# Optimization experiments

Hardware: AMD Instinct MI355X
Metric: run time of the kernel (lower is better)

The kernel has to match this reference:

```python
import jax, jax.numpy as jnp
import numpy as np

B, N, E = 8, 4096, 131072
F_IN, F_OUT = 64, 64
ALPHA = 0.2  # LeakyReLU negative slope


def setup_inputs() -> dict:
    key = jax.random.key(0)
    k1, k2, k3, k4, k5 = jax.random.split(key, 5)
    h = jax.random.normal(k1, (B, N, F_IN), dtype=jnp.float32)
    edge_index = jax.random.randint(k2, (2, E), 0, N)
    edge_weight = jax.random.uniform(k3, (E,), dtype=jnp.float32)
    # learned params: Linear weight (no bias) and attention vector a (2*F_OUT, 1)
    W = jax.random.normal(k4, (F_IN, F_OUT), dtype=jnp.float32) / np.sqrt(F_IN)
    a = jax.random.normal(k5, (2 * F_OUT, 1), dtype=jnp.float32) * 0.1
    return {"h": h, "edge_index": edge_index, "edge_weight": edge_weight, "W": W, "a": a}


def _gat_forward(h, edge_weight, W, a, src, dst):
    # Wh: (B, N, F')
    Wh = jnp.einsum("bnf,fo->bno", h, W)
    a1, a2 = a[:F_OUT, 0], a[F_OUT:, 0]
    # score decomposition: [Wh_src || Wh_dst] @ a == Wh_src@a1 + Wh_dst@a2
    s_src = Wh @ a1  # (B, N)
    s_dst = Wh @ a2  # (B, N)
    e = s_src[:, src] + s_dst[:, dst]           # (B, E)
    e = jnp.where(e > 0, e, ALPHA * e)          # LeakyReLU
    e = e * edge_weight[None, :]
    # sparse row-softmax over dst, grouped by src (equals dense masked softmax)
    eT = e.T                                     # (E, B)
    m = jax.ops.segment_max(eT, src, num_segments=N)   # (N, B)
    m = jnp.where(jnp.isfinite(m), m, 0.0)       # rows with no edges
    ex = jnp.exp(eT - m[src])                    # (E, B)
    denom = jax.ops.segment_sum(ex, src, num_segments=N)  # (N, B)
    attn = ex / denom[src]                       # (E, B); denom>0 wherever an edge exists
    # aggregate: h'[b, i] = sum_{e: src[e]=i} attn[e,b] * Wh[b, dst[e]]
    msg = attn[:, :, None] * jnp.transpose(Wh[:, dst], (1, 0, 2))  # (E, B, F')
    hp = jax.ops.segment_sum(msg, src, num_segments=N)             # (N, B, F')
    hp = jnp.transpose(hp, (1, 0, 2))            # (B, N, F')
    return jnp.where(hp > 0, hp, jnp.expm1(hp))  # ELU


def reference(h, edge_index, edge_weight, W, a):
    src, dst = edge_index[0], edge_index[1]
    return _gat_forward(h, edge_weight, W, a, src, dst)
```

## Files before the change

### kernel.cpp

```cpp
#include <hip/hip_runtime.h>
#include <math.h>

#define NB 8
#define NN 4096
#define NE 131072
#define NF 64
#define CAP 256
#define PCAP 128
#define LRELU_ALPHA 0.2f

static __device__ __forceinline__ ushort bf16r(float x) {
  uint u = __float_as_uint(x);
  return (ushort)((u + 0x7fffu + ((u >> 16) & 1u)) >> 16);
}

__global__ __launch_bounds__(256) void fused_gemm_append_kernel(
    const float* __restrict__ h, const float* __restrict__ W,
    const float* __restrict__ a, const int* __restrict__ src,
    const int* __restrict__ dst, const float* __restrict__ ew,
    ushort* __restrict__ Whb, float* __restrict__ ssrc,
    float* __restrict__ sdst, int* __restrict__ cnt,
    int2* __restrict__ bucket) {
  int tid = threadIdx.x;
  int blk = blockIdx.x;
  if (blk >= 512) {
    int e = (blk - 512) * 256 + tid;
    int s = src[e];
    int d = dst[e];
    float w = ew[e];
    int p = atomicAdd(&cnt[s], 1);
    if (p < CAP) bucket[s * CAP + p] = make_int2(d, __float_as_int(w));
    return;
  }
  int f = tid & 63;
  int wave = blk * 4 + (tid >> 6);
  float Wc[64];
#pragma unroll
  for (int k = 0; k < 64; k++) Wc[k] = W[k * 64 + f];
  float A1 = a[f];
  float A2 = a[64 + f];

  int row0 = __builtin_amdgcn_readfirstlane(wave) * 16;
#pragma unroll 2
  for (int r = 0; r < 16; r++) {
    int row = row0 + r;
    const float* hr = h + (size_t)row * NF;
    float ac0 = 0.f, ac1 = 0.f, ac2 = 0.f, ac3 = 0.f;
#pragma unroll
    for (int k = 0; k < 64; k += 4) {
      ac0 += hr[k] * Wc[k];
      ac1 += hr[k + 1] * Wc[k + 1];
      ac2 += hr[k + 2] * Wc[k + 2];
      ac3 += hr[k + 3] * Wc[k + 3];
    }
    float acc = (ac0 + ac1) + (ac2 + ac3);
    Whb[(size_t)row * NF + f] = bf16r(acc);
    float v1 = acc * A1;
    float v2 = acc * A2;
#pragma unroll
    for (int off = 1; off < 64; off <<= 1) {
      v1 += __shfl_xor(v1, off);
      v2 += __shfl_xor(v2, off);
    }
    if (f == 0) ssrc[row] = v1;
    if (f == 32) sdst[row] = v2;
  }
}

__global__ __launch_bounds__(512) void agg_kernel(
    const ushort* __restrict__ Whb, const float* __restrict__ ssrc,
    const float* __restrict__ sdst, const int* __restrict__ cnt,
    const int2* __restrict__ bucket, float* __restrict__ out) {
  __shared__ int2 pex[8][PCAP];
  int blk = blockIdx.x;
  int b = blk & 7;
  int g = blk >> 3;
  int tid = threadIdx.x;
  int w = tid >> 6;
  int f = tid & 63;
  int n = g * 8 + w;

  int cntn = min(cnt[n], PCAP);
  float ss = ssrc[b * NN + n];
  const float* sdB = sdst + b * NN;
  const int2* bkt = bucket + n * CAP;
  float den = 0.f;
  for (int i = f; i < cntn; i += 64) {
    int2 e = bkt[i];
    float x = ss + sdB[e.x];
    x = (x > 0.f) ? x : LRELU_ALPHA * x;
    x *= __int_as_float(e.y);
    float v = __expf(x);
    pex[w][i] = make_int2(e.x, __float_as_int(v));
    den += v;
  }
#pragma unroll
  for (int off = 1; off < 64; off <<= 1) den += __shfl_xor(den, off);

  const ushort* WhB = Whb + (size_t)b * NN * NF;
  const int4* pv = (const int4*)&pex[w][0];
  float acc0 = 0.f, acc1 = 0.f, acc2 = 0.f, acc3 = 0.f;
  float acc4 = 0.f, acc5 = 0.f, acc6 = 0.f, acc7 = 0.f;
  int i = 0;
  for (; i + 8 <= cntn; i += 8) {
    int4 q0 = pv[(i >> 1) + 0];
    int4 q1 = pv[(i >> 1) + 1];
    int4 q2 = pv[(i >> 1) + 2];
    int4 q3 = pv[(i >> 1) + 3];
    float w0 = __uint_as_float(((uint)WhB[(q0.x << 6) + f]) << 16);
    float w1 = __uint_as_float(((uint)WhB[(q0.z << 6) + f]) << 16);
    float w2 = __uint_as_float(((uint)WhB[(q1.x << 6) + f]) << 16);
    float w3 = __uint_as_float(((uint)WhB[(q1.z << 6) + f]) << 16);
    float w4 = __uint_as_float(((uint)WhB[(q2.x << 6) + f]) << 16);
    float w5 = __uint_as_float(((uint)WhB[(q2.z << 6) + f]) << 16);
    float w6 = __uint_as_float(((uint)WhB[(q3.x << 6) + f]) << 16);
    float w7 = __uint_as_float(((uint)WhB[(q3.z << 6) + f]) << 16);
    acc0 += __int_as_float(q0.y) * w0;
    acc1 += __int_as_float(q0.w) * w1;
    acc2 += __int_as_float(q1.y) * w2;
    acc3 += __int_as_float(q1.w) * w3;
    acc4 += __int_as_float(q2.y) * w4;
    acc5 += __int_as_float(q2.w) * w5;
    acc6 += __int_as_float(q3.y) * w6;
    acc7 += __int_as_float(q3.w) * w7;
  }
  for (; i < cntn; i++) {
    int2 p = pex[w][i];
    acc0 += __int_as_float(p.y) *
            __uint_as_float(((uint)WhB[(p.x << 6) + f]) << 16);
  }
  float accs = ((acc0 + acc1) + (acc2 + acc3)) + ((acc4 + acc5) + (acc6 + acc7));
  float hp = (cntn > 0) ? accs / den : 0.f;
  out[((size_t)(b * NN + n)) * NF + f] = (hp > 0.f) ? hp : expm1f(hp);
}

extern "C" void kernel_launch(void* const* d_in, const int* in_sizes, int n_in,
                              void* d_out, int out_size, void* d_ws,
                              size_t ws_size, hipStream_t stream) {
  const float* h = (const float*)d_in[0];
  const int* edge_index = (const int*)d_in[1];
  const float* ew = (const float*)d_in[2];
  const float* W = (const float*)d_in[3];
  const float* a = (const float*)d_in[4];
  float* out = (float*)d_out;

  const int* src = edge_index;
  const int* dst = edge_index + NE;

  uint8_t* ws = (uint8_t*)d_ws;
  ushort* Whb = (ushort*)ws;
  float* ssrc = (float*)(ws + 4194304);
  float* sdst = (float*)(ws + 4325376);
  int* cnt = (int*)(ws + 4456448);
  int2* bucket = (int2*)(ws + 4472832);

  hipMemsetAsync(cnt, 0, NN * sizeof(int), stream);
  fused_gemm_append_kernel<<<1024, 256, 0, stream>>>(h, W, a, src, dst, ew,
                                                     Whb, ssrc, sdst, cnt,
                                                     bucket);
  agg_kernel<<<NN, 512, 0, stream>>>(Whb, ssrc, sdst, cnt, bucket, out);
}
```

Measured before the change: 117.6 us.

## Interleave Wh by batch per node so aggregation processes all batches per edge

```diff
diff --git a/kernel.cpp b/kernel.cpp
--- a/kernel.cpp
+++ b/kernel.cpp
@@ -13,6 +13,12 @@
   uint u = __float_as_uint(x);
   return (ushort)((u + 0x7fffu + ((u >> 16) & 1u)) >> 16);
 }
+static __device__ __forceinline__ float bflo(int u) {
+  return __uint_as_float(((uint)u) << 16);
+}
+static __device__ __forceinline__ float bfhi(int u) {
+  return __uint_as_float(((uint)u) & 0xffff0000u);
+}
 
 __global__ __launch_bounds__(256) void fused_gemm_append_kernel(
     const float* __restrict__ h, const float* __restrict__ W,
@@ -23,8 +29,8 @@
     int2* __restrict__ bucket) {
   int tid = threadIdx.x;
   int blk = blockIdx.x;
-  if (blk >= 512) {
-    int e = (blk - 512) * 256 + tid;
+  if (blk >= 1024) {
+    int e = (blk - 1024) * 256 + tid;
     int s = src[e];
     int d = dst[e];
     float w = ew[e];
@@ -40,9 +46,11 @@
   float A1 = a[f];
   float A2 = a[64 + f];
 
-  int row0 = __builtin_amdgcn_readfirstlane(wave) * 16;
+  int row0 = __builtin_amdgcn_readfirstlane(wave) * 8;
+  int b = row0 >> 12;
+  int nb = row0 & 4095;
 #pragma unroll 2
-  for (int r = 0; r < 16; r++) {
+  for (int r = 0; r < 8; r++) {
     int row = row0 + r;
     const float* hr = h + (size_t)row * NF;
     float ac0 = 0.f, ac1 = 0.f, ac2 = 0.f, ac3 = 0.f;
@@ -54,7 +62,8 @@
       ac3 += hr[k + 3] * Wc[k + 3];
     }
     float acc = (ac0 + ac1) + (ac2 + ac3);
-    Whb[(size_t)row * NF + f] = bf16r(acc);
+    int n8b = (nb + r) * 8 + b;
+    Whb[(size_t)n8b * NF + f] = bf16r(acc);
     float v1 = acc * A1;
     float v2 = acc * A2;
 #pragma unroll
@@ -62,76 +71,102 @@
       v1 += __shfl_xor(v1, off);
       v2 += __shfl_xor(v2, off);
     }
-    if (f == 0) ssrc[row] = v1;
-    if (f == 32) sdst[row] = v2;
+    if (f == 0) ssrc[n8b] = v1;
+    if (f == 32) sdst[n8b] = v2;
   }
 }
 
-__global__ __launch_bounds__(512) void agg_kernel(
+__global__ __launch_bounds__(256) void agg_kernel(
     const ushort* __restrict__ Whb, const float* __restrict__ ssrc,
     const float* __restrict__ sdst, const int* __restrict__ cnt,
     const int2* __restrict__ bucket, float* __restrict__ out) {
-  __shared__ int2 pex[8][PCAP];
-  int blk = blockIdx.x;
-  int b = blk & 7;
-  int g = blk >> 3;
+  __shared__ float pexv[4][PCAP * 8];
+  __shared__ int dste[4][PCAP];
   int tid = threadIdx.x;
   int w = tid >> 6;
-  int f = tid & 63;
-  int n = g * 8 + w;
+  int l = tid & 63;
+  int n = blockIdx.x * 4 + w;
+  int cntn = min(cnt[n], PCAP);
 
-  int cntn = min(cnt[n], PCAP);
-  float ss = ssrc[b * NN + n];
-  const float* sdB = sdst + b * NN;
+  int es = l >> 3;
+  int b1 = l & 7;
+  float ss = ssrc[n * 8 + b1];
   const int2* bkt = bucket + n * CAP;
   float den = 0.f;
-  for (int i = f; i < cntn; i += 64) {
-    int2 e = bkt[i];
-    float x = ss + sdB[e.x];
-    x = (x > 0.f) ? x : LRELU_ALPHA * x;
-    x *= __int_as_float(e.y);
-    float v = __expf(x);
-    pex[w][i] = make_int2(e.x, __float_as_int(v));
-    den += v;
+  for (int e0 = 0; e0 < cntn; e0 += 8) {
+    int e = e0 + es;
+    if (e < cntn) {
+      int2 ed = bkt[e];
+      float x = ss + sdst[ed.x * 8 + b1];
+      x = (x > 0.f) ? x : LRELU_ALPHA * x;
+      x *= __int_as_float(ed.y);
+      float v = __expf(x);
+      pexv[w][e * 8 + b1] = v;
+      if (b1 == 0) dste[w][e] = ed.x;
+      den += v;
+    }
   }
-#pragma unroll
-  for (int off = 1; off < 64; off <<= 1) den += __shfl_xor(den, off);
+  den += __shfl_xor(den, 8);
+  den += __shfl_xor(den, 16);
+  den += __shfl_xor(den, 32);
 
-  const ushort* WhB = Whb + (size_t)b * NN * NF;
-  const int4* pv = (const int4*)&pex[w][0];
+  int b2 = l >> 3;
+  int fi = l & 7;
+  float dn = __shfl(den, b2);
+  const ushort* wp = Whb + l * 8;
   float acc0 = 0.f, acc1 = 0.f, acc2 = 0.f, acc3 = 0.f;
   float acc4 = 0.f, acc5 = 0.f, acc6 = 0.f, acc7 = 0.f;
-  int i = 0;
-  for (; i + 8 <= cntn; i += 8) {
-    int4 q0 = pv[(i >> 1) + 0];
-    int4 q1 = pv[(i >> 1) + 1];
-    int4 q2 = pv[(i >> 1) + 2];
-    int4 q3 = pv[(i >> 1) + 3];
-    float w0 = __uint_as_float(((uint)WhB[(q0.x << 6) + f]) << 16);
-    float w1 = __uint_as_float(((uint)WhB[(q0.z << 6) + f]) << 16);
-    float w2 = __uint_as_float(((uint)WhB[(q1.x << 6) + f]) << 16);
-    float w3 = __uint_as_float(((uint)WhB[(q1.z << 6) + f]) << 16);
-    float w4 = __uint_as_float(((uint)WhB[(q2.x << 6) + f]) << 16);
-    float w5 = __uint_as_float(((uint)WhB[(q2.z << 6) + f]) << 16);
-    float w6 = __uint_as_float(((uint)WhB[(q3.x << 6) + f]) << 16);
-    float w7 = __uint_as_float(((uint)WhB[(q3.z << 6) + f]) << 16);
-    acc0 += __int_as_float(q0.y) * w0;
-    acc1 += __int_as_float(q0.w) * w1;
-    acc2 += __int_as_float(q1.y) * w2;
-    acc3 += __int_as_float(q1.w) * w3;
-    acc4 += __int_as_float(q2.y) * w4;
-    acc5 += __int_as_float(q2.w) * w5;
-    acc6 += __int_as_float(q3.y) * w6;
-    acc7 += __int_as_float(q3.w) * w7;
+  int e = 0;
+  for (; e + 4 <= cntn; e += 4) {
+    int4 dd = *(const int4*)&dste[w][e];
+    float ev0 = pexv[w][(e + 0) * 8 + b2];
+    float ev1 = pexv[w][(e + 1) * 8 + b2];
+    float ev2 = pexv[w][(e + 2) * 8 + b2];
+    float ev3 = pexv[w][(e + 3) * 8 + b2];
+    int4 q0 = *(const int4*)(wp + (size_t)dd.x * 512);
+    int4 q1 = *(const int4*)(wp + (size_t)dd.y * 512);
+    int4 q2 = *(const int4*)(wp + (size_t)dd.z * 512);
+    int4 q3 = *(const int4*)(wp + (size_t)dd.w * 512);
+    acc0 += ev0 * bflo(q0.x); acc1 += ev0 * bfhi(q0.x);
+    acc2 += ev0 * bflo(q0.y); acc3 += ev0 * bfhi(q0.y);
+    acc4 += ev0 * bflo(q0.z); acc5 += ev0 * bfhi(q0.z);
+    acc6 += ev0 * bflo(q0.w); acc7 += ev0 * bfhi(q0.w);
+    acc0 += ev1 * bflo(q1.x); acc1 += ev1 * bfhi(q1.x);
+    acc2 += ev1 * bflo(q1.y); acc3 += ev1 * bfhi(q1.y);
+    acc4 += ev1 * bflo(q1.z); acc5 += ev1 * bfhi(q1.z);
+    acc6 += ev1 * bflo(q1.w); acc7 += ev1 * bfhi(q1.w);
+    acc0 += ev2 * bflo(q2.x); acc1 += ev2 * bfhi(q2.x);
+    acc2 += ev2 * bflo(q2.y); acc3 += ev2 * bfhi(q2.y);
+    acc4 += ev2 * bflo(q2.z); acc5 += ev2 * bfhi(q2.z);
+    acc6 += ev2 * bflo(q2.w); acc7 += ev2 * bfhi(q2.w);
+    acc0 += ev3 * bflo(q3.x); acc1 += ev3 * bfhi(q3.x);
+    acc2 += ev3 * bflo(q3.y); acc3 += ev3 * bfhi(q3.y);
+    acc4 += ev3 * bflo(q3.z); acc5 += ev3 * bfhi(q3.z);
+    acc6 += ev3 * bflo(q3.w); acc7 += ev3 * bfhi(q3.w);
   }
-  for (; i < cntn; i++) {
-    int2 p = pex[w][i];
-    acc0 += __int_as_float(p.y) *
-            __uint_as_float(((uint)WhB[(p.x << 6) + f]) << 16);
+  for (; e < cntn; e++) {
+    int d = dste[w][e];
+    float ev = pexv[w][e * 8 + b2];
+    int4 q = *(const int4*)(wp + (size_t)d * 512);
+    acc0 += ev * bflo(q.x); acc1 += ev * bfhi(q.x);
+    acc2 += ev * bflo(q.y); acc3 += ev * bfhi(q.y);
+    acc4 += ev * bflo(q.z); acc5 += ev * bfhi(q.z);
+    acc6 += ev * bflo(q.w); acc7 += ev * bfhi(q.w);
   }
-  float accs = ((acc0 + acc1) + (acc2 + acc3)) + ((acc4 + acc5) + (acc6 + acc7));
-  float hp = (cntn > 0) ? accs / den : 0.f;
-  out[((size_t)(b * NN + n)) * NF + f] = (hp > 0.f) ? hp : expm1f(hp);
+  float inv = (cntn > 0) ? (1.0f / dn) : 0.f;
+  float r0 = acc0 * inv, r1 = acc1 * inv, r2 = acc2 * inv, r3 = acc3 * inv;
+  float r4 = acc4 * inv, r5 = acc5 * inv, r6 = acc6 * inv, r7 = acc7 * inv;
+  r0 = (r0 > 0.f) ? r0 : expm1f(r0);
+  r1 = (r1 > 0.f) ? r1 : expm1f(r1);
+  r2 = (r2 > 0.f) ? r2 : expm1f(r2);
+  r3 = (r3 > 0.f) ? r3 : expm1f(r3);
+  r4 = (r4 > 0.f) ? r4 : expm1f(r4);
+  r5 = (r5 > 0.f) ? r5 : expm1f(r5);
+  r6 = (r6 > 0.f) ? r6 : expm1f(r6);
+  r7 = (r7 > 0.f) ? r7 : expm1f(r7);
+  size_t ob = ((size_t)(b2 * NN + n)) * NF + fi * 8;
+  *(float4*)(out + ob) = make_float4(r0, r1, r2, r3);
+  *(float4*)(out + ob + 4) = make_float4(r4, r5, r6, r7);
 }
 
 extern "C" void kernel_launch(void* const* d_in, const int* in_sizes, int n_in,
@@ -155,8 +190,8 @@
   int2* bucket = (int2*)(ws + 4472832);
 
   hipMemsetAsync(cnt, 0, NN * sizeof(int), stream);
-  fused_gemm_append_kernel<<<1024, 256, 0, stream>>>(h, W, a, src, dst, ew,
+  fused_gemm_append_kernel<<<1536, 256, 0, stream>>>(h, W, a, src, dst, ew,
                                                      Whb, ssrc, sdst, cnt,
                                                      bucket);
-  agg_kernel<<<NN, 512, 0, stream>>>(Whb, ssrc, sdst, cnt, bucket, out);
+  agg_kernel<<<NN / 4, 256, 0, stream>>>(Whb, ssrc, sdst, cnt, bucket, out);
 }
```

Result: faster. 100.7 us (-14.4%).
